# Kernel tuning notes

Hardware: AMD Instinct MI355X
Metric: run time of the kernel (lower is better)

## Reference

```python
import jax, jax.numpy as jnp
import numpy as np


def setup_inputs() -> dict:
    key = jax.random.key(0)
    k1, k2, k3, k4, k5 = jax.random.split(key, 5)
    S, B, He, Hd, A = 2048, 32, 1024, 1024, 512
    dec_out = jax.random.normal(k1, (B, Hd), dtype=jnp.float32)
    enc_outs = jax.random.normal(k2, (S, B, He), dtype=jnp.float32)
    # parameter scales matching nn.Linear default init (~U(-1/sqrt(fan_in), ...))
    W_enc = jax.random.normal(k3, (A, He), dtype=jnp.float32) / np.sqrt(He)
    W_dec = jax.random.normal(k4, (A, Hd), dtype=jnp.float32) / np.sqrt(Hd)
    att_v = jax.random.normal(k5, (A,), dtype=jnp.float32) / np.sqrt(A)
    return {"dec_out": dec_out, "enc_outs": enc_outs, "W_enc": W_enc,
            "W_dec": W_dec, "att_v": att_v}


def reference(dec_out, enc_outs, W_enc, W_dec, att_v):
    # enc_att: (S, B, A) = enc_outs @ W_enc^T
    enc_att = jnp.einsum('sbh,ah->sba', enc_outs, W_enc)
    # dec_att: (B, A) = dec_out @ W_dec^T, tiled over seq_len
    dec_att = jnp.einsum('bh,ah->ba', dec_out, W_dec)
    # additive score: tanh(enc_att + dec_att) . att_v  -> (B, S)
    dec_enc_att = jnp.tanh(enc_att + dec_att[None, :, :])      # (S, B, A)
    scores = jnp.einsum('sba,a->bs', dec_enc_att, att_v)       # (B, S)
    weights = jax.nn.softmax(scores, axis=-1)                  # (B, S)
    # context: weighted sum of encoder outputs -> (B, He)
    context = jnp.einsum('bs,sbh->bh', weights, enc_outs)
    return context, weights
```

## Files before the change

### kernel.cpp

```cpp
#include <hip/hip_runtime.h>
#include <hip/hip_bf16.h>


typedef float f32x4 __attribute__((ext_vector_type(4)));
typedef __bf16 bf16x8 __attribute__((ext_vector_type(8)));

#define WS_DEC_OFF    0u
#define WS_WIMG_OFF   65536u
#define WS_PART_OFF   (65536u + 1048576u)
#define WS_SPART_OFF  WS_PART_OFF

__device__ __forceinline__ void gload_lds16(const void* g, void* l) {
  __builtin_amdgcn_global_load_lds(
      (const __attribute__((address_space(1))) void*)g,
      (__attribute__((address_space(3))) void*)l, 16, 0, 0);
}

__global__ void dec_att_kernel(const float* __restrict__ dec_out,
                               const float* __restrict__ W_dec,
                               float* __restrict__ out) {
  int gtid = blockIdx.x * blockDim.x + threadIdx.x;
  int w = gtid >> 6;
  int lane = gtid & 63;
  int b = w >> 9;
  int a = w & 511;
  const float4* dp = (const float4*)(dec_out + b * 1024);
  const float4* wp = (const float4*)(W_dec + a * 1024);
  float sum = 0.f;
#pragma unroll
  for (int i = 0; i < 4; ++i) {
    float4 x = dp[lane + i * 64];
    float4 y = wp[lane + i * 64];
    sum += x.x * y.x + x.y * y.y + x.z * y.z + x.w * y.w;
  }
#pragma unroll
  for (int m = 32; m; m >>= 1) sum += __shfl_xor(sum, m, 64);
  if (lane == 0) out[b * 512 + a] = sum;
}

__global__ void convert_wenc(const float* __restrict__ W, __bf16* __restrict__ out) {
  int idx = blockIdx.x * 256 + threadIdx.x;
  int t = idx >> 14;
  int r = (idx >> 5) & 511;
  int s = (idx >> 3) & 3;
  int e = idx & 7;
  out[idx] = (__bf16)W[r * 1024 + t * 32 + ((s ^ (r & 3)) << 3) + e];
}

__global__ __launch_bounds__(256, 2) void scores_gemm(
    const float* __restrict__ enc,
    const __bf16* __restrict__ wimg,
    const float* __restrict__ dec_att,
    const float* __restrict__ attv,
    float* __restrict__ spart) {
  __shared__ __align__(16) char smem[25600];

  const int tid = threadIdx.x;
  const int lane = tid & 63;
  const int w = tid >> 6;
  const int wr = w >> 1;
  const int wn = w & 1;
  const int q = lane >> 4;
  const int c0 = lane & 15;

  const int xcd = blockIdx.x & 7;
  const int idx = blockIdx.x >> 3;
  const int bm = xcd + ((idx >> 2) << 3);
  const int nb = idx & 3;

  f32x4 acc[4][4];
#pragma unroll
  for (int i = 0; i < 4; ++i)
#pragma unroll
    for (int j = 0; j < 4; ++j) acc[i][j] = (f32x4){0.f, 0.f, 0.f, 0.f};

  const int j_a = (tid & 7) ^ ((tid >> 3) & 7);
  const float* abase = enc + ((size_t)(bm * 128 + (tid >> 3))) * 1024 + j_a * 4;
  const char* bimg = (const char*)wimg;

  int a_off[4][2], b_off[4];
#pragma unroll
  for (int mf = 0; mf < 4; ++mf) {
    const int rl = wr * 64 + mf * 16 + c0;
#pragma unroll
    for (int j = 0; j < 2; ++j)
      a_off[mf][j] = rl * 128 + (((2 * q + j) ^ (rl & 7)) << 4);
  }
#pragma unroll
  for (int nf = 0; nf < 4; ++nf) {
    const int rn = wn * 64 + nf * 16 + c0;
    b_off[nf] = 16384 + rn * 64 + ((q ^ (rn & 3)) << 4);
  }

  for (int t = 0; t < 32; ++t) {
#pragma unroll
    for (int p = 0; p < 4; ++p)
      gload_lds16(abase + t * 32 + p * 32768, smem + p * 4096 + tid * 16);
    {
      const char* bs = bimg + (size_t)t * 32768 + nb * 8192 + tid * 16;
      gload_lds16(bs, smem + 16384 + tid * 16);
      gload_lds16(bs + 4096, smem + 16384 + 4096 + tid * 16);
    }
    __syncthreads();

    bf16x8 af[4], bfr[4];
#pragma unroll
    for (int mf = 0; mf < 4; ++mf) {
      f32x4 u0 = *(const f32x4*)(smem + a_off[mf][0]);
      f32x4 u1 = *(const f32x4*)(smem + a_off[mf][1]);
      bf16x8 v;
      v[0] = (__bf16)u0[0]; v[1] = (__bf16)u0[1]; v[2] = (__bf16)u0[2]; v[3] = (__bf16)u0[3];
      v[4] = (__bf16)u1[0]; v[5] = (__bf16)u1[1]; v[6] = (__bf16)u1[2]; v[7] = (__bf16)u1[3];
      af[mf] = v;
    }
#pragma unroll
    for (int nf = 0; nf < 4; ++nf) bfr[nf] = *(const bf16x8*)(smem + b_off[nf]);
#pragma unroll
    for (int mf = 0; mf < 4; ++mf)
#pragma unroll
      for (int nf = 0; nf < 4; ++nf)
        acc[mf][nf] = __builtin_amdgcn_mfma_f32_16x16x32_bf16(af[mf], bfr[nf],
                                                              acc[mf][nf], 0, 0, 0);
    __syncthreads();
  }

  float* epart = (float*)(smem + 24576);
  float av[4];
#pragma unroll
  for (int nf = 0; nf < 4; ++nf) av[nf] = attv[nb * 128 + wn * 64 + nf * 16 + c0];

#pragma unroll
  for (int mf = 0; mf < 4; ++mf) {
#pragma unroll
    for (int rg = 0; rg < 4; ++rg) {
      const int rl = wr * 64 + mf * 16 + q * 4 + rg;
      const int b = rl & 31;
      const float* drow = dec_att + b * 512 + nb * 128 + wn * 64 + c0;
      float sum = 0.f;
#pragma unroll
      for (int nf = 0; nf < 4; ++nf) {
        float x = acc[mf][nf][rg] + drow[nf * 16];
        float e = __expf(2.f * x);
        float th = 1.f - 2.f / (e + 1.f);
        sum += th * av[nf];
      }
      sum += __shfl_xor(sum, 1, 64);
      sum += __shfl_xor(sum, 2, 64);
      sum += __shfl_xor(sum, 4, 64);
      sum += __shfl_xor(sum, 8, 64);
      if (c0 == 0) epart[rl * 2 + wn] = sum;
    }
  }
  __syncthreads();
  if (tid < 128) {
    float tot = epart[tid * 2] + epart[tid * 2 + 1];
    spart[nb * 65536 + (tid & 31) * 2048 + bm * 4 + (tid >> 5)] = tot;
  }
}

__global__ void softmax_kernel(const float* __restrict__ spart,
                               float* __restrict__ weights) {
  const int b = blockIdx.x;
  const int t = threadIdx.x;
  const float4* p0 = (const float4*)(spart + b * 2048);
  const float4* p1 = (const float4*)(spart + 65536 + b * 2048);
  const float4* p2 = (const float4*)(spart + 131072 + b * 2048);
  const float4* p3 = (const float4*)(spart + 196608 + b * 2048);
  float4 v0, v1;
  {
    float4 a0 = p0[t], a1 = p1[t], a2 = p2[t], a3 = p3[t];
    v0.x = a0.x + a1.x + a2.x + a3.x; v0.y = a0.y + a1.y + a2.y + a3.y;
    v0.z = a0.z + a1.z + a2.z + a3.z; v0.w = a0.w + a1.w + a2.w + a3.w;
    a0 = p0[t + 256]; a1 = p1[t + 256]; a2 = p2[t + 256]; a3 = p3[t + 256];
    v1.x = a0.x + a1.x + a2.x + a3.x; v1.y = a0.y + a1.y + a2.y + a3.y;
    v1.z = a0.z + a1.z + a2.z + a3.z; v1.w = a0.w + a1.w + a2.w + a3.w;
  }
  float mx = fmaxf(fmaxf(fmaxf(v0.x, v0.y), fmaxf(v0.z, v0.w)),
                   fmaxf(fmaxf(v1.x, v1.y), fmaxf(v1.z, v1.w)));
#pragma unroll
  for (int s = 32; s; s >>= 1) mx = fmaxf(mx, __shfl_xor(mx, s, 64));
  __shared__ float redm[4], reds[4];
  if ((t & 63) == 0) redm[t >> 6] = mx;
  __syncthreads();
  mx = fmaxf(fmaxf(redm[0], redm[1]), fmaxf(redm[2], redm[3]));
  float4 e0, e1;
  e0.x = __expf(v0.x - mx); e0.y = __expf(v0.y - mx);
  e0.z = __expf(v0.z - mx); e0.w = __expf(v0.w - mx);
  e1.x = __expf(v1.x - mx); e1.y = __expf(v1.y - mx);
  e1.z = __expf(v1.z - mx); e1.w = __expf(v1.w - mx);
  float s8 = e0.x + e0.y + e0.z + e0.w + e1.x + e1.y + e1.z + e1.w;
#pragma unroll
  for (int s = 32; s; s >>= 1) s8 += __shfl_xor(s8, s, 64);
  if ((t & 63) == 0) reds[t >> 6] = s8;
  __syncthreads();
  float inv = 1.f / (reds[0] + reds[1] + reds[2] + reds[3]);
  e0.x *= inv; e0.y *= inv; e0.z *= inv; e0.w *= inv;
  e1.x *= inv; e1.y *= inv; e1.z *= inv; e1.w *= inv;
  float4* wrow = (float4*)(weights + b * 2048);
  wrow[t] = e0;
  wrow[t + 256] = e1;
}

__global__ void ctx_partial(const float* __restrict__ enc,
                            const float* __restrict__ weights,
                            float* __restrict__ part) {
  const int b = blockIdx.x & 31;
  const int sc = blockIdx.x >> 5;
  const int t = threadIdx.x;
  const float* wrow = weights + b * 2048 + sc * 128;
  const char* ebase = (const char*)(enc + ((size_t)(sc * 128) * 32 + b) * 1024) + t * 16;
  float4 acc = {0.f, 0.f, 0.f, 0.f};
#pragma unroll 4
  for (int i = 0; i < 128; ++i) {
    float4 e = *(const float4*)(ebase + (size_t)i * 131072);
    float ws = wrow[i];
    acc.x += ws * e.x; acc.y += ws * e.y; acc.z += ws * e.z; acc.w += ws * e.w;
  }
  *(float4*)(part + (size_t)(sc * 32 + b) * 1024 + t * 4) = acc;
}

__global__ void ctx_reduce(const float* __restrict__ part, float* __restrict__ ctx) {
  int idx = blockIdx.x * 256 + threadIdx.x;
  float s = 0.f;
#pragma unroll
  for (int c = 0; c < 16; ++c) s += part[c * 32768 + idx];
  ctx[idx] = s;
}

extern "C" void kernel_launch(void* const* d_in, const int* in_sizes, int n_in,
                              void* d_out, int out_size, void* d_ws, size_t ws_size,
                              hipStream_t stream) {
  const float* dec_out  = (const float*)d_in[0];
  const float* enc_outs = (const float*)d_in[1];
  const float* W_enc    = (const float*)d_in[2];
  const float* W_dec    = (const float*)d_in[3];
  const float* att_v    = (const float*)d_in[4];

  float* out = (float*)d_out;
  float* ctx = out;
  float* weights = out + 32768;

  char* ws = (char*)d_ws;
  float*  ws_dec    = (float*)(ws + WS_DEC_OFF);
  __bf16* ws_wimg   = (__bf16*)(ws + WS_WIMG_OFF);
  float*  ws_spart  = (float*)(ws + WS_SPART_OFF);
  float*  ws_part   = (float*)(ws + WS_PART_OFF);

  dec_att_kernel<<<4096, 256, 0, stream>>>(dec_out, W_dec, ws_dec);
  convert_wenc<<<2048, 256, 0, stream>>>(W_enc, ws_wimg);
  scores_gemm<<<2048, 256, 0, stream>>>(enc_outs, ws_wimg, ws_dec, att_v, ws_spart);
  softmax_kernel<<<32, 256, 0, stream>>>(ws_spart, weights);
  ctx_partial<<<512, 256, 0, stream>>>(enc_outs, weights, ws_part);
  ctx_reduce<<<128, 256, 0, stream>>>(ws_part, ctx);
}
```

Baseline: 169.2 us.

## Double-buffer scores GEMM loads and reuse bf16 encoder copy for context

The scores GEMM now double-buffers the A and B tiles in LDS, prefetching the next K-slice while the current one runs on MFMA. It uses explicit vmcnt waits and raw barriers and raises the occupancy hint to 3. When the workspace is large enough, one wave group per M tile also writes the bf16-converted encoder fragments to a 128 MB workspace buffer. The context kernel then reads that bf16 copy instead of the fp32 input, halving the traffic of the second pass over encoder outputs. In exchange the GEMM does extra global writes, uses more LDS, and the context sum is computed from bf16-rounded activations, which lowers accuracy.

Result: slower. 201.9 us (+19.4%).

```diff
diff --git a/kernel.cpp b/kernel.cpp
--- a/kernel.cpp
+++ b/kernel.cpp
@@ -9,6 +9,8 @@
 #define WS_WIMG_OFF   65536u
 #define WS_PART_OFF   (65536u + 1048576u)
 #define WS_SPART_OFF  WS_PART_OFF
+#define WS_ENCB_OFF   4194304u
+#define WS_NEED_BIG   (4194304ull + 134217728ull)
 
 __device__ __forceinline__ void gload_lds16(const void* g, void* l) {
   __builtin_amdgcn_global_load_lds(
@@ -47,13 +49,15 @@
   out[idx] = (__bf16)W[r * 1024 + t * 32 + ((s ^ (r & 3)) << 3) + e];
 }
 
-__global__ __launch_bounds__(256, 2) void scores_gemm(
+template <int WBF>
+__global__ __launch_bounds__(256, 3) void scores_gemm(
     const float* __restrict__ enc,
     const __bf16* __restrict__ wimg,
     const float* __restrict__ dec_att,
     const float* __restrict__ attv,
-    float* __restrict__ spart) {
-  __shared__ __align__(16) char smem[25600];
+    float* __restrict__ spart,
+    __bf16* __restrict__ encb) {
+  __shared__ __align__(16) char smem[50176];
 
   const int tid = threadIdx.x;
   const int lane = tid & 63;
@@ -76,7 +80,7 @@
 
   const int j_a = (tid & 7) ^ ((tid >> 3) & 7);
   const float* abase = enc + ((size_t)(bm * 128 + (tid >> 3))) * 1024 + j_a * 4;
-  const char* bimg = (const char*)wimg;
+  const char* bsrc0 = (const char*)wimg + nb * 8192 + tid * 16;
 
   int a_off[4][2], b_off[4];
 #pragma unroll
@@ -89,42 +93,69 @@
 #pragma unroll
   for (int nf = 0; nf < 4; ++nf) {
     const int rn = wn * 64 + nf * 16 + c0;
-    b_off[nf] = 16384 + rn * 64 + ((q ^ (rn & 3)) << 4);
-  }
+    b_off[nf] = rn * 64 + ((q ^ (rn & 3)) << 4);
+  }
+
+  {
+#pragma unroll
+    for (int p = 0; p < 4; ++p)
+      gload_lds16(abase + p * 32768, smem + p * 4096 + tid * 16);
+    gload_lds16(bsrc0, smem + 32768 + tid * 16);
+    gload_lds16(bsrc0 + 4096, smem + 32768 + 4096 + tid * 16);
+    asm volatile("s_waitcnt vmcnt(0)" ::: "memory");
+  }
+  __builtin_amdgcn_s_barrier();
 
   for (int t = 0; t < 32; ++t) {
-#pragma unroll
-    for (int p = 0; p < 4; ++p)
-      gload_lds16(abase + t * 32 + p * 32768, smem + p * 4096 + tid * 16);
-    {
-      const char* bs = bimg + (size_t)t * 32768 + nb * 8192 + tid * 16;
-      gload_lds16(bs, smem + 16384 + tid * 16);
-      gload_lds16(bs + 4096, smem + 16384 + 4096 + tid * 16);
+    const int cur = t & 1;
+    if (t < 31) {
+      const int d = cur ^ 1;
+#pragma unroll
+      for (int p = 0; p < 4; ++p)
+        gload_lds16(abase + (t + 1) * 32 + p * 32768,
+                    smem + d * 16384 + p * 4096 + tid * 16);
+      const char* bs = bsrc0 + (size_t)(t + 1) * 32768;
+      gload_lds16(bs, smem + 32768 + d * 8192 + tid * 16);
+      gload_lds16(bs + 4096, smem + 32768 + d * 8192 + 4096 + tid * 16);
+      if (WBF && nb == 0 && wn == 0)
+        asm volatile("s_waitcnt vmcnt(10)" ::: "memory");
+      else
+        asm volatile("s_waitcnt vmcnt(6)" ::: "memory");
+    } else {
+      asm volatile("s_waitcnt vmcnt(0)" ::: "memory");
     }
-    __syncthreads();
-
+    __builtin_amdgcn_s_barrier();
+
+    char* ab = smem + cur * 16384;
+    char* bb = smem + 32768 + cur * 8192;
     bf16x8 af[4], bfr[4];
 #pragma unroll
     for (int mf = 0; mf < 4; ++mf) {
-      f32x4 u0 = *(const f32x4*)(smem + a_off[mf][0]);
-      f32x4 u1 = *(const f32x4*)(smem + a_off[mf][1]);
+      f32x4 u0 = *(const f32x4*)(ab + a_off[mf][0]);
+      f32x4 u1 = *(const f32x4*)(ab + a_off[mf][1]);
       bf16x8 v;
       v[0] = (__bf16)u0[0]; v[1] = (__bf16)u0[1]; v[2] = (__bf16)u0[2]; v[3] = (__bf16)u0[3];
       v[4] = (__bf16)u1[0]; v[5] = (__bf16)u1[1]; v[6] = (__bf16)u1[2]; v[7] = (__bf16)u1[3];
       af[mf] = v;
     }
 #pragma unroll
-    for (int nf = 0; nf < 4; ++nf) bfr[nf] = *(const bf16x8*)(smem + b_off[nf]);
+    for (int nf = 0; nf < 4; ++nf) bfr[nf] = *(const bf16x8*)(bb + b_off[nf]);
 #pragma unroll
     for (int mf = 0; mf < 4; ++mf)
 #pragma unroll
       for (int nf = 0; nf < 4; ++nf)
         acc[mf][nf] = __builtin_amdgcn_mfma_f32_16x16x32_bf16(af[mf], bfr[nf],
                                                               acc[mf][nf], 0, 0, 0);
-    __syncthreads();
-  }
-
-  float* epart = (float*)(smem + 24576);
+    if (WBF && nb == 0 && wn == 0) {
+#pragma unroll
+      for (int mf = 0; mf < 4; ++mf)
+        *(bf16x8*)(encb + ((size_t)(bm * 128 + wr * 64 + mf * 16 + c0)) * 1024 +
+                   t * 32 + q * 8) = af[mf];
+    }
+    __builtin_amdgcn_s_barrier();
+  }
+
+  float* epart = (float*)(smem + 49152);
   float av[4];
 #pragma unroll
   for (int nf = 0; nf < 4; ++nf) av[nf] = attv[nb * 128 + wn * 64 + nf * 16 + c0];
@@ -219,6 +250,27 @@
   *(float4*)(part + (size_t)(sc * 32 + b) * 1024 + t * 4) = acc;
 }
 
+__global__ void ctx_partial_bf16(const __bf16* __restrict__ encb,
+                                 const float* __restrict__ weights,
+                                 float* __restrict__ part) {
+  const int b = blockIdx.x & 31;
+  const int sc = blockIdx.x >> 5;
+  const int t = threadIdx.x;
+  const float* wrow = weights + b * 2048 + sc * 128;
+  const __bf16* ebase = encb + ((size_t)(sc * 128) * 32 + b) * 1024 + t * 8;
+  float acc[8] = {0.f, 0.f, 0.f, 0.f, 0.f, 0.f, 0.f, 0.f};
+#pragma unroll 4
+  for (int i = 0; i < 128; ++i) {
+    bf16x8 e = *(const bf16x8*)(ebase + (size_t)i * 32768);
+    float ws = wrow[i];
+#pragma unroll
+    for (int j = 0; j < 8; ++j) acc[j] += ws * (float)e[j];
+  }
+  float* dst = part + (size_t)(sc * 32 + b) * 1024 + t * 8;
+#pragma unroll
+  for (int j = 0; j < 8; ++j) dst[j] = acc[j];
+}
+
 __global__ void ctx_reduce(const float* __restrict__ part, float* __restrict__ ctx) {
   int idx = blockIdx.x * 256 + threadIdx.x;
   float s = 0.f;
@@ -245,11 +297,22 @@
   __bf16* ws_wimg   = (__bf16*)(ws + WS_WIMG_OFF);
   float*  ws_spart  = (float*)(ws + WS_SPART_OFF);
   float*  ws_part   = (float*)(ws + WS_PART_OFF);
+  __bf16* ws_encb   = (__bf16*)(ws + WS_ENCB_OFF);
+
+  const bool big = ws_size >= WS_NEED_BIG;
 
   dec_att_kernel<<<4096, 256, 0, stream>>>(dec_out, W_dec, ws_dec);
   convert_wenc<<<2048, 256, 0, stream>>>(W_enc, ws_wimg);
-  scores_gemm<<<2048, 256, 0, stream>>>(enc_outs, ws_wimg, ws_dec, att_v, ws_spart);
-  softmax_kernel<<<32, 256, 0, stream>>>(ws_spart, weights);
-  ctx_partial<<<512, 256, 0, stream>>>(enc_outs, weights, ws_part);
+  if (big) {
+    scores_gemm<1><<<2048, 256, 0, stream>>>(enc_outs, ws_wimg, ws_dec, att_v,
+                                             ws_spart, ws_encb);
+    softmax_kernel<<<32, 256, 0, stream>>>(ws_spart, weights);
+    ctx_partial_bf16<<<512, 128, 0, stream>>>(ws_encb, weights, ws_part);
+  } else {
+    scores_gemm<0><<<2048, 256, 0, stream>>>(enc_outs, ws_wimg, ws_dec, att_v,
+                                             ws_spart, ws_encb);
+    softmax_kernel<<<32, 256, 0, stream>>>(ws_spart, weights);
+    ctx_partial<<<512, 256, 0, stream>>>(enc_outs, weights, ws_part);
+  }
   ctx_reduce<<<128, 256, 0, stream>>>(ws_part, ctx);
 }
```

## Software-pipeline scores GEMM with register-staged A and double-buffered LDS

Applied to the files above, without the earlier changes.

The A tile of encoder outputs is now loaded from global memory into registers two iterations ahead, converted to bf16 once per thread and written to a double-buffered bf16 LDS area. The B tile is prefetched one iteration ahead with global_load_lds into a second buffer. This replaces the fp32 LDS staging and the two syncthreads per iteration with a single barrier and manual waitcnts, so loads overlap the MFMAs and the bf16 conversion is no longer repeated across waves. It also raises the occupancy hint to 3 blocks and adds setprio around the MFMAs. The cost is more LDS and higher register pressure, and the hand-written vmcnt counts must stay correct.

Result: slower. 205.4 us (+21.4%).

```diff
diff --git a/kernel.cpp b/kernel.cpp
--- a/kernel.cpp
+++ b/kernel.cpp
@@ -47,13 +47,13 @@
   out[idx] = (__bf16)W[r * 1024 + t * 32 + ((s ^ (r & 3)) << 3) + e];
 }
 
-__global__ __launch_bounds__(256, 2) void scores_gemm(
+__global__ __launch_bounds__(256, 3) void scores_gemm(
     const float* __restrict__ enc,
     const __bf16* __restrict__ wimg,
     const float* __restrict__ dec_att,
     const float* __restrict__ attv,
     float* __restrict__ spart) {
-  __shared__ __align__(16) char smem[25600];
+  __shared__ __align__(16) char smem[33792];
 
   const int tid = threadIdx.x;
   const int lane = tid & 63;
@@ -74,17 +74,18 @@
 #pragma unroll
     for (int j = 0; j < 4; ++j) acc[i][j] = (f32x4){0.f, 0.f, 0.f, 0.f};
 
-  const int j_a = (tid & 7) ^ ((tid >> 3) & 7);
-  const float* abase = enc + ((size_t)(bm * 128 + (tid >> 3))) * 1024 + j_a * 4;
-  const char* bimg = (const char*)wimg;
-
-  int a_off[4][2], b_off[4];
+  const int srow = tid >> 1;
+  const int kh = tid & 1;
+  const float* asrc = enc + ((size_t)(bm * 128 + srow)) * 1024 + kh * 16;
+  const int aw0 = srow * 64 + (((2 * kh) ^ (srow & 3)) << 4);
+  const int aw1 = srow * 64 + (((2 * kh + 1) ^ (srow & 3)) << 4);
+  const char* bsrc0 = (const char*)wimg + nb * 8192 + tid * 16;
+
+  int a_off[4], b_off[4];
 #pragma unroll
   for (int mf = 0; mf < 4; ++mf) {
     const int rl = wr * 64 + mf * 16 + c0;
-#pragma unroll
-    for (int j = 0; j < 2; ++j)
-      a_off[mf][j] = rl * 128 + (((2 * q + j) ^ (rl & 7)) << 4);
+    a_off[mf] = rl * 64 + ((q ^ (rl & 3)) << 4);
   }
 #pragma unroll
   for (int nf = 0; nf < 4; ++nf) {
@@ -92,39 +93,67 @@
     b_off[nf] = 16384 + rn * 64 + ((q ^ (rn & 3)) << 4);
   }
 
+  float4 aP0, aP1, aP2, aP3, aQ0, aQ1, aQ2, aQ3;
+
+#define LOAD_A(dst0, dst1, dst2, dst3, t)                         \
+  { const float4* s4 = (const float4*)(asrc + (t) * 32);          \
+    dst0 = s4[0]; dst1 = s4[1]; dst2 = s4[2]; dst3 = s4[3]; }
+
+#define CVT_WRITE_A(buf, s0, s1, s2, s3)                                        \
+  { bf16x8 v0, v1;                                                              \
+    v0[0] = (__bf16)s0.x; v0[1] = (__bf16)s0.y; v0[2] = (__bf16)s0.z;           \
+    v0[3] = (__bf16)s0.w; v0[4] = (__bf16)s1.x; v0[5] = (__bf16)s1.y;           \
+    v0[6] = (__bf16)s1.z; v0[7] = (__bf16)s1.w;                                 \
+    v1[0] = (__bf16)s2.x; v1[1] = (__bf16)s2.y; v1[2] = (__bf16)s2.z;           \
+    v1[3] = (__bf16)s2.w; v1[4] = (__bf16)s3.x; v1[5] = (__bf16)s3.y;           \
+    v1[6] = (__bf16)s3.z; v1[7] = (__bf16)s3.w;                                 \
+    *(bf16x8*)(smem + (buf) * 8192 + aw0) = v0;                                 \
+    *(bf16x8*)(smem + (buf) * 8192 + aw1) = v1; }
+
+  LOAD_A(aP0, aP1, aP2, aP3, 0);
+  LOAD_A(aQ0, aQ1, aQ2, aQ3, 1);
+  gload_lds16(bsrc0, smem + 16384 + tid * 16);
+  gload_lds16(bsrc0 + 4096, smem + 16384 + 4096 + tid * 16);
+  asm volatile("s_waitcnt vmcnt(6)" ::: "memory");
+  CVT_WRITE_A(0, aP0, aP1, aP2, aP3);
+  asm volatile("s_waitcnt lgkmcnt(0)" ::: "memory");
+  __builtin_amdgcn_s_barrier();
+
   for (int t = 0; t < 32; ++t) {
-#pragma unroll
-    for (int p = 0; p < 4; ++p)
-      gload_lds16(abase + t * 32 + p * 32768, smem + p * 4096 + tid * 16);
+    const int cur = t & 1;
     {
-      const char* bs = bimg + (size_t)t * 32768 + nb * 8192 + tid * 16;
-      gload_lds16(bs, smem + 16384 + tid * 16);
-      gload_lds16(bs + 4096, smem + 16384 + 4096 + tid * 16);
+      const int ta = (t + 2 > 31) ? 31 : t + 2;
+      const int tb = (t + 1 > 31) ? 31 : t + 1;
+      if (cur == 0) { LOAD_A(aP0, aP1, aP2, aP3, ta); }
+      else          { LOAD_A(aQ0, aQ1, aQ2, aQ3, ta); }
+      const char* bs = bsrc0 + (size_t)tb * 32768;
+      char* bd = smem + 16384 + (cur ^ 1) * 4096 * 2;
+      gload_lds16(bs, bd + tid * 16);
+      gload_lds16(bs + 4096, bd + 4096 + tid * 16);
     }
-    __syncthreads();
-
+    asm volatile("s_waitcnt vmcnt(6)" ::: "memory");
+    if (cur == 0) { CVT_WRITE_A(1, aQ0, aQ1, aQ2, aQ3); }
+    else          { CVT_WRITE_A(0, aP0, aP1, aP2, aP3); }
     bf16x8 af[4], bfr[4];
 #pragma unroll
-    for (int mf = 0; mf < 4; ++mf) {
-      f32x4 u0 = *(const f32x4*)(smem + a_off[mf][0]);
-      f32x4 u1 = *(const f32x4*)(smem + a_off[mf][1]);
-      bf16x8 v;
-      v[0] = (__bf16)u0[0]; v[1] = (__bf16)u0[1]; v[2] = (__bf16)u0[2]; v[3] = (__bf16)u0[3];
-      v[4] = (__bf16)u1[0]; v[5] = (__bf16)u1[1]; v[6] = (__bf16)u1[2]; v[7] = (__bf16)u1[3];
-      af[mf] = v;
-    }
-#pragma unroll
-    for (int nf = 0; nf < 4; ++nf) bfr[nf] = *(const bf16x8*)(smem + b_off[nf]);
+    for (int mf = 0; mf < 4; ++mf)
+      af[mf] = *(const bf16x8*)(smem + cur * 8192 + a_off[mf]);
+#pragma unroll
+    for (int nf = 0; nf < 4; ++nf)
+      bfr[nf] = *(const bf16x8*)(smem + cur * 8192 + b_off[nf]);
+    __builtin_amdgcn_s_setprio(1);
 #pragma unroll
     for (int mf = 0; mf < 4; ++mf)
 #pragma unroll
       for (int nf = 0; nf < 4; ++nf)
         acc[mf][nf] = __builtin_amdgcn_mfma_f32_16x16x32_bf16(af[mf], bfr[nf],
                                                               acc[mf][nf], 0, 0, 0);
-    __syncthreads();
-  }
-
-  float* epart = (float*)(smem + 24576);
+    __builtin_amdgcn_s_setprio(0);
+    asm volatile("s_waitcnt lgkmcnt(0)" ::: "memory");
+    __builtin_amdgcn_s_barrier();
+  }
+
+  float* epart = (float*)(smem + 32768);
   float av[4];
 #pragma unroll
   for (int nf = 0; nf < 4; ++nf) av[nf] = attv[nb * 128 + wn * 64 + nf * 16 + c0];
@@ -156,6 +185,8 @@
     float tot = epart[tid * 2] + epart[tid * 2 + 1];
     spart[nb * 65536 + (tid & 31) * 2048 + bm * 4 + (tid >> 5)] = tot;
   }
+#undef LOAD_A
+#undef CVT_WRITE_A
 }
 
 __global__ void softmax_kernel(const float* __restrict__ spart,
```

## Retile scores GEMM to 64x256 with double-buffered LDS and register-prefetched A

Applied to the files above, without the earlier changes.

Changes the scores GEMM tile from 128 rows x 128 attention cols to 64 rows x 256 cols, so each block covers half the attention dimension and the number of N-partials drops from four to two. The fp32 encoder tile is now loaded into registers one K-step ahead, converted to bf16 once, and written to a double-buffered LDS A tile. The B tile is double-buffered via async global-to-LDS loads, with one barrier per iteration, and MFMA priority is raised. The W_enc image layout and the softmax partial reduction are updated to match, and occupancy is raised to 3 blocks per CU at the cost of more LDS per block.

Measured after the change: 174.7 us. +3.3%, slower.

```diff
diff --git a/kernel.cpp b/kernel.cpp
--- a/kernel.cpp
+++ b/kernel.cpp
@@ -40,33 +40,31 @@
 
 __global__ void convert_wenc(const float* __restrict__ W, __bf16* __restrict__ out) {
   int idx = blockIdx.x * 256 + threadIdx.x;
-  int t = idx >> 14;
-  int r = (idx >> 5) & 511;
-  int s = (idx >> 3) & 3;
-  int e = idx & 7;
-  out[idx] = (__bf16)W[r * 1024 + t * 32 + ((s ^ (r & 3)) << 3) + e];
-}
-
-__global__ __launch_bounds__(256, 2) void scores_gemm(
+  int kc = idx >> 14;
+  int q = (idx >> 12) & 3;
+  int row = (idx >> 3) & 511;
+  int j = idx & 7;
+  out[idx] = (__bf16)W[row * 1024 + kc * 32 + q * 8 + j];
+}
+
+__global__ __launch_bounds__(256, 3) void scores_gemm(
     const float* __restrict__ enc,
     const __bf16* __restrict__ wimg,
     const float* __restrict__ dec_att,
     const float* __restrict__ attv,
     float* __restrict__ spart) {
-  __shared__ __align__(16) char smem[25600];
+  __shared__ __align__(16) char smem[41984];
 
   const int tid = threadIdx.x;
   const int lane = tid & 63;
   const int w = tid >> 6;
-  const int wr = w >> 1;
-  const int wn = w & 1;
   const int q = lane >> 4;
   const int c0 = lane & 15;
 
   const int xcd = blockIdx.x & 7;
   const int idx = blockIdx.x >> 3;
-  const int bm = xcd + ((idx >> 2) << 3);
-  const int nb = idx & 3;
+  const int bm = xcd + ((idx >> 1) << 3);
+  const int nb = idx & 1;
 
   f32x4 acc[4][4];
 #pragma unroll
@@ -74,68 +72,87 @@
 #pragma unroll
     for (int j = 0; j < 4; ++j) acc[i][j] = (f32x4){0.f, 0.f, 0.f, 0.f};
 
-  const int j_a = (tid & 7) ^ ((tid >> 3) & 7);
-  const float* abase = enc + ((size_t)(bm * 128 + (tid >> 3))) * 1024 + j_a * 4;
-  const char* bimg = (const char*)wimg;
-
-  int a_off[4][2], b_off[4];
+  const int srow = tid >> 2;
+  const int sq = tid & 3;
+  const float* asrc = enc + (size_t)(bm * 64 + srow) * 1024 + sq * 8;
+  const int a_woff = srow * 64 + (((sq ^ (srow & 3)) << 4));
+
+  const char* bsrc = (const char*)wimg + (tid >> 6) * 8192 + nb * 4096 + (tid & 63) * 16;
+  const int b_dst = (tid >> 6) * 4096 + (tid & 63) * 16;
+
+  int a_off[4], b_off[4];
 #pragma unroll
   for (int mf = 0; mf < 4; ++mf) {
-    const int rl = wr * 64 + mf * 16 + c0;
-#pragma unroll
-    for (int j = 0; j < 2; ++j)
-      a_off[mf][j] = rl * 128 + (((2 * q + j) ^ (rl & 7)) << 4);
+    const int rl = mf * 16 + c0;
+    a_off[mf] = rl * 64 + ((q ^ (rl & 3)) << 4);
   }
 #pragma unroll
   for (int nf = 0; nf < 4; ++nf) {
-    const int rn = wn * 64 + nf * 16 + c0;
-    b_off[nf] = 16384 + rn * 64 + ((q ^ (rn & 3)) << 4);
-  }
+    const int rn = w * 64 + nf * 16 + c0;
+    b_off[nf] = q * 4096 + rn * 16;
+  }
+
+  {
+    const float4* s4 = (const float4*)asrc;
+    float4 x = s4[0], y = s4[1];
+#pragma unroll
+    for (int p = 0; p < 4; ++p)
+      gload_lds16(bsrc + p * 1024, smem + 8192 + b_dst + p * 1024);
+    bf16x8 v;
+    v[0] = (__bf16)x.x; v[1] = (__bf16)x.y; v[2] = (__bf16)x.z; v[3] = (__bf16)x.w;
+    v[4] = (__bf16)y.x; v[5] = (__bf16)y.y; v[6] = (__bf16)y.z; v[7] = (__bf16)y.w;
+    *(bf16x8*)(smem + a_woff) = v;
+  }
+  __syncthreads();
 
   for (int t = 0; t < 32; ++t) {
-#pragma unroll
-    for (int p = 0; p < 4; ++p)
-      gload_lds16(abase + t * 32 + p * 32768, smem + p * 4096 + tid * 16);
-    {
-      const char* bs = bimg + (size_t)t * 32768 + nb * 8192 + tid * 16;
-      gload_lds16(bs, smem + 16384 + tid * 16);
-      gload_lds16(bs + 4096, smem + 16384 + 4096 + tid * 16);
+    const int cur = t & 1;
+    float4 nx, ny;
+    if (t < 31) {
+      const float4* s4 = (const float4*)(asrc + (t + 1) * 32);
+      nx = s4[0]; ny = s4[1];
+      const char* bs = bsrc + (size_t)(t + 1) * 32768;
+      char* bd = smem + 8192 + (cur ^ 1) * 16384 + b_dst;
+#pragma unroll
+      for (int p = 0; p < 4; ++p)
+        gload_lds16(bs + p * 1024, bd + p * 1024);
     }
-    __syncthreads();
-
     bf16x8 af[4], bfr[4];
 #pragma unroll
-    for (int mf = 0; mf < 4; ++mf) {
-      f32x4 u0 = *(const f32x4*)(smem + a_off[mf][0]);
-      f32x4 u1 = *(const f32x4*)(smem + a_off[mf][1]);
-      bf16x8 v;
-      v[0] = (__bf16)u0[0]; v[1] = (__bf16)u0[1]; v[2] = (__bf16)u0[2]; v[3] = (__bf16)u0[3];
-      v[4] = (__bf16)u1[0]; v[5] = (__bf16)u1[1]; v[6] = (__bf16)u1[2]; v[7] = (__bf16)u1[3];
-      af[mf] = v;
-    }
-#pragma unroll
-    for (int nf = 0; nf < 4; ++nf) bfr[nf] = *(const bf16x8*)(smem + b_off[nf]);
+    for (int mf = 0; mf < 4; ++mf)
+      af[mf] = *(const bf16x8*)(smem + cur * 4096 + a_off[mf]);
+#pragma unroll
+    for (int nf = 0; nf < 4; ++nf)
+      bfr[nf] = *(const bf16x8*)(smem + 8192 + cur * 16384 + b_off[nf]);
+    __builtin_amdgcn_s_setprio(1);
 #pragma unroll
     for (int mf = 0; mf < 4; ++mf)
 #pragma unroll
       for (int nf = 0; nf < 4; ++nf)
         acc[mf][nf] = __builtin_amdgcn_mfma_f32_16x16x32_bf16(af[mf], bfr[nf],
                                                               acc[mf][nf], 0, 0, 0);
+    __builtin_amdgcn_s_setprio(0);
+    if (t < 31) {
+      bf16x8 v;
+      v[0] = (__bf16)nx.x; v[1] = (__bf16)nx.y; v[2] = (__bf16)nx.z; v[3] = (__bf16)nx.w;
+      v[4] = (__bf16)ny.x; v[5] = (__bf16)ny.y; v[6] = (__bf16)ny.z; v[7] = (__bf16)ny.w;
+      *(bf16x8*)(smem + (cur ^ 1) * 4096 + a_woff) = v;
+    }
     __syncthreads();
   }
 
-  float* epart = (float*)(smem + 24576);
+  float* epart = (float*)(smem + 40960);
   float av[4];
 #pragma unroll
-  for (int nf = 0; nf < 4; ++nf) av[nf] = attv[nb * 128 + wn * 64 + nf * 16 + c0];
+  for (int nf = 0; nf < 4; ++nf) av[nf] = attv[nb * 256 + w * 64 + nf * 16 + c0];
 
 #pragma unroll
   for (int mf = 0; mf < 4; ++mf) {
 #pragma unroll
     for (int rg = 0; rg < 4; ++rg) {
-      const int rl = wr * 64 + mf * 16 + q * 4 + rg;
+      const int rl = mf * 16 + q * 4 + rg;
       const int b = rl & 31;
-      const float* drow = dec_att + b * 512 + nb * 128 + wn * 64 + c0;
+      const float* drow = dec_att + b * 512 + nb * 256 + w * 64 + c0;
       float sum = 0.f;
 #pragma unroll
       for (int nf = 0; nf < 4; ++nf) {
@@ -148,13 +165,14 @@
       sum += __shfl_xor(sum, 2, 64);
       sum += __shfl_xor(sum, 4, 64);
       sum += __shfl_xor(sum, 8, 64);
-      if (c0 == 0) epart[rl * 2 + wn] = sum;
+      if (c0 == 0) epart[rl * 4 + w] = sum;
     }
   }
   __syncthreads();
-  if (tid < 128) {
-    float tot = epart[tid * 2] + epart[tid * 2 + 1];
-    spart[nb * 65536 + (tid & 31) * 2048 + bm * 4 + (tid >> 5)] = tot;
+  if (tid < 64) {
+    float tot = epart[tid * 4] + epart[tid * 4 + 1] +
+                epart[tid * 4 + 2] + epart[tid * 4 + 3];
+    spart[nb * 65536 + (tid & 31) * 2048 + bm * 2 + (tid >> 5)] = tot;
   }
 }
 
@@ -164,16 +182,12 @@
   const int t = threadIdx.x;
   const float4* p0 = (const float4*)(spart + b * 2048);
   const float4* p1 = (const float4*)(spart + 65536 + b * 2048);
-  const float4* p2 = (const float4*)(spart + 131072 + b * 2048);
-  const float4* p3 = (const float4*)(spart + 196608 + b * 2048);
   float4 v0, v1;
   {
-    float4 a0 = p0[t], a1 = p1[t], a2 = p2[t], a3 = p3[t];
-    v0.x = a0.x + a1.x + a2.x + a3.x; v0.y = a0.y + a1.y + a2.y + a3.y;
-    v0.z = a0.z + a1.z + a2.z + a3.z; v0.w = a0.w + a1.w + a2.w + a3.w;
-    a0 = p0[t + 256]; a1 = p1[t + 256]; a2 = p2[t + 256]; a3 = p3[t + 256];
-    v1.x = a0.x + a1.x + a2.x + a3.x; v1.y = a0.y + a1.y + a2.y + a3.y;
-    v1.z = a0.z + a1.z + a2.z + a3.z; v1.w = a0.w + a1.w + a2.w + a3.w;
+    float4 a0 = p0[t], a1 = p1[t];
+    v0.x = a0.x + a1.x; v0.y = a0.y + a1.y; v0.z = a0.z + a1.z; v0.w = a0.w + a1.w;
+    a0 = p0[t + 256]; a1 = p1[t + 256];
+    v1.x = a0.x + a1.x; v1.y = a0.y + a1.y; v1.z = a0.z + a1.z; v1.w = a0.w + a1.w;
   }
   float mx = fmaxf(fmaxf(fmaxf(v0.x, v0.y), fmaxf(v0.z, v0.w)),
                    fmaxf(fmaxf(v1.x, v1.y), fmaxf(v1.z, v1.w)));
```
